# Kernel tuning notes

Measured on AMD Instinct MI355X. Metric: run time of the kernel, lower is better.

The kernel has to match this reference:

```python
import jax, jax.numpy as jnp
import numpy as np

B, T, N = 128, 32, 196
E = 1024   # embed dim
FD = 1024  # feature dim
H = 1024   # hidden size
A = 1024   # attention dim
SCALE = 0.02


def setup_inputs() -> dict:
    key = jax.random.key(0)
    ks = jax.random.split(key, 16)
    g = lambda k, shape: (jax.random.normal(k, shape, dtype=jnp.float32) * SCALE)
    return {
        "feats": jax.random.normal(ks[0], (B, N, FD), dtype=jnp.float32),
        "embeddings": jax.random.normal(ks[1], (B, T, E), dtype=jnp.float32),
        # additive attention params: v^T tanh(feats @ Wf + h @ Wh + b_att)
        "Wf": g(ks[2], (FD, A)),
        "Wh": g(ks[3], (H, A)),
        "b_att": jnp.zeros((A,), dtype=jnp.float32),
        "v": g(ks[4], (A,)),
        # layer-0 LSTMCell (input = concat(embed, attn) of size E+FD)
        "W_ih0": g(ks[5], (4 * H, E + FD)),
        "W_hh0": g(ks[6], (4 * H, H)),
        "b_ih0": jnp.zeros((4 * H,), dtype=jnp.float32),
        "b_hh0": jnp.zeros((4 * H,), dtype=jnp.float32),
        # layer-1 LSTMCell (input size H)
        "W_ih1": g(ks[7], (4 * H, H)),
        "W_hh1": g(ks[8], (4 * H, H)),
        "b_ih1": jnp.zeros((4 * H,), dtype=jnp.float32),
        "b_hh1": jnp.zeros((4 * H,), dtype=jnp.float32),
    }


def _lstm_cell(x, h, c, W_ih, W_hh, b_ih, b_hh):
    # PyTorch LSTMCell: gates ordered i, f, g, o
    gates = x @ W_ih.T + h @ W_hh.T + (b_ih + b_hh)
    i, f, g, o = jnp.split(gates, 4, axis=-1)
    c_new = jax.nn.sigmoid(f) * c + jax.nn.sigmoid(i) * jnp.tanh(g)
    h_new = jax.nn.sigmoid(o) * jnp.tanh(c_new)
    return h_new, c_new


def reference(feats, embeddings, Wf, Wh, b_att, v, W_ih0, W_hh0, b_ih0, b_hh0,
              W_ih1, W_hh1, b_ih1, b_hh1):
    Bb = embeddings.shape[0]
    # precompute the h-independent half of the attention energies: [B, N, A]
    f_proj = jnp.einsum("bnf,fa->bna", feats, Wf) + b_att

    h0 = jnp.zeros((Bb, H), dtype=feats.dtype)
    c0 = jnp.zeros((Bb, H), dtype=feats.dtype)

    def step(carry, embed_t):
        h0, c0 = carry
        # additive attention with query h0
        e = jnp.tanh(f_proj + (h0 @ Wh)[:, None, :])      # [B, N, A]
        scores = jnp.einsum("bna,a->bn", e, v)            # [B, N]
        alpha = jax.nn.softmax(scores, axis=-1)
        attn = jnp.einsum("bn,bnf->bf", alpha, feats)     # [B, FD]
        x = jnp.concatenate([embed_t, attn], axis=1)      # [B, E+FD]
        h0n, c0n = _lstm_cell(x, h0, c0, W_ih0, W_hh0, b_ih0, b_hh0)
        # faithful to source: layer 1 uses (h0n, c0n) as its state AND h0n as input
        h1, c1 = _lstm_cell(h0n, h0n, c0n, W_ih1, W_hh1, b_ih1, b_hh1)
        return (h0n, c0n), h1

    (_, _), outs = jax.lax.scan(step, (h0, c0), jnp.swapaxes(embeddings, 0, 1))
    return jnp.swapaxes(outs, 0, 1)  # [B, T, H]
```

## Files before the change

### kernel.cpp

```cpp
#include <hip/hip_runtime.h>
#include <hip/hip_cooperative_groups.h>
#include <cstddef>

typedef unsigned short ushort_t;
typedef unsigned int uint_t;
typedef __attribute__((ext_vector_type(8))) short bf16x8;
typedef __attribute__((ext_vector_type(4))) float f32x4;

constexpr int kB  = 128;
constexpr int kT  = 32;
constexpr int kN  = 196;
constexpr int kH  = 1024;

constexpr int ARENA_BYTES = 34816;

__device__ __forceinline__ float fsigmoid(float x) { return 1.f / (1.f + __expf(-x)); }
__device__ __forceinline__ float ftanh(float x)    { return 1.f - 2.f / (__expf(2.f * x) + 1.f); }
__device__ __forceinline__ ushort_t f2bf(float f) {
    uint_t u = __float_as_uint(f);
    return (ushort_t)((u + 0x7fffu + ((u >> 16) & 1u)) >> 16);
}

__global__ __launch_bounds__(256) void wf_transpose(
    const float* __restrict__ Wsrc, ushort_t* __restrict__ dst)
{
    __shared__ float t[64][65];
    const int k0 = blockIdx.x * 64, a0 = blockIdx.y * 64;
    const int c = threadIdx.x & 15, r0 = threadIdx.x >> 4;
#pragma unroll
    for (int i = 0; i < 4; ++i) {
        const int r = r0 + i * 16;
        const float4 v = *(const float4*)(Wsrc + (size_t)(k0 + r) * 1024 + a0 + c * 4);
        t[r][c * 4 + 0] = v.x; t[r][c * 4 + 1] = v.y;
        t[r][c * 4 + 2] = v.z; t[r][c * 4 + 3] = v.w;
    }
    __syncthreads();
#pragma unroll
    for (int i = 0; i < 4; ++i) {
        const int r = r0 + i * 16;
        ushort4 h;
        h.x = f2bf(t[c * 4 + 0][r]); h.y = f2bf(t[c * 4 + 1][r]);
        h.z = f2bf(t[c * 4 + 2][r]); h.w = f2bf(t[c * 4 + 3][r]);
        *(ushort4*)&dst[(size_t)(a0 + r) * 1024 + k0 + c * 4] = h;
    }
}

__global__ __launch_bounds__(256) void pack_whh0(
    const float* __restrict__ Whh0, ushort_t* __restrict__ Wbig)
{
    const int idx = blockIdx.x * 256 + threadIdx.x;
    const int j = idx >> 8, k4 = (idx & 255) * 4;
    const int u = j >> 2, g = j & 3;
    const float4 v = *(const float4*)(Whh0 + (size_t)(g * 1024 + u) * 1024 + k4);
    ushort4 h;
    h.x = f2bf(v.x); h.y = f2bf(v.y); h.z = f2bf(v.z); h.w = f2bf(v.w);
    *(ushort4*)&Wbig[(size_t)(1024 + j) * 1024 + k4] = h;
}

__global__ __launch_bounds__(256) void pack_w1sum(
    const float* __restrict__ Wih1, const float* __restrict__ Whh1,
    ushort_t* __restrict__ Wbig)
{
    const int idx = blockIdx.x * 256 + threadIdx.x;
    const int j = idx >> 8, k4 = (idx & 255) * 4;
    const int u = j >> 2, g = j & 3;
    const size_t o = (size_t)(g * 1024 + u) * 1024 + k4;
    const float4 a = *(const float4*)(Wih1 + o);
    const float4 b = *(const float4*)(Whh1 + o);
    ushort4 h;
    h.x = f2bf(a.x + b.x); h.y = f2bf(a.y + b.y);
    h.z = f2bf(a.z + b.z); h.w = f2bf(a.w + b.w);
    *(ushort4*)&Wbig[(size_t)(5120 + j) * 1024 + k4] = h;
}

__global__ __launch_bounds__(256) void pack_w0cat(
    const float* __restrict__ Wih0, ushort_t* __restrict__ W0cat)
{
    const int idx = blockIdx.x * 256 + threadIdx.x;
    const int j = idx >> 9, k4 = (idx & 511) * 4;
    const int u = j >> 2, g = j & 3;
    const int srccol = (k4 < 1024) ? (k4 + 1024) : (k4 - 1024);
    const float4 v = *(const float4*)(Wih0 + (size_t)(g * 1024 + u) * 2048 + srccol);
    ushort4 h;
    h.x = f2bf(v.x); h.y = f2bf(v.y); h.z = f2bf(v.z); h.w = f2bf(v.w);
    *(ushort4*)&W0cat[(size_t)j * 2048 + k4] = h;
}

__global__ __launch_bounds__(256) void cast_bf(
    const float* __restrict__ src, ushort_t* __restrict__ dst)
{
    const size_t idx = ((size_t)blockIdx.x * 256 + threadIdx.x) * 4;
    const float4 v = *(const float4*)(src + idx);
    ushort4 h;
    h.x = f2bf(v.x); h.y = f2bf(v.y); h.z = f2bf(v.z); h.w = f2bf(v.w);
    *(ushort4*)&dst[idx] = h;
}

template<int BF>
__global__ __launch_bounds__(256) void fproj_mfma(
    const float* __restrict__ featsf, const ushort_t* __restrict__ featsbf,
    const ushort_t* __restrict__ WfT,
    const float* __restrict__ bias, ushort_t* __restrict__ fprojbf)
{
    __shared__ alignas(16) char farena[40960];
    ushort_t* As = (ushort_t*)farena;
    ushort_t* Bs = As + 2 * 5120;
    ushort_t* Cs = (ushort_t*)farena;

    const int tid = threadIdx.x;
    const int n0 = blockIdx.x * 128, m0 = blockIdx.y * 128;
    const int lane = tid & 63, w = tid >> 6;
    const int wm = (w & 1) * 64, wn = (w >> 1) * 64;
    const int lr = lane & 15, quad = lane >> 4;

    const int xrow0 = tid >> 2, xrow1 = 64 + (tid >> 2);
    const int xkc = (tid & 3) * 8;

    f32x4 acc[4][4];
#pragma unroll
    for (int i = 0; i < 4; ++i)
#pragma unroll
        for (int j = 0; j < 4; ++j)
            acc[i][j] = (f32x4){0.f, 0.f, 0.f, 0.f};

    uint4 a0r, a1r, b0r, b1r;
    float4 f00, f01, f10, f11;

    auto LOAD = [&](int k0) {
        if (BF) {
            a0r = *(const uint4*)&featsbf[(size_t)(m0 + xrow0) * 1024 + k0 + xkc];
            a1r = *(const uint4*)&featsbf[(size_t)(m0 + xrow1) * 1024 + k0 + xkc];
        } else {
            f00 = *(const float4*)&featsf[(size_t)(m0 + xrow0) * 1024 + k0 + xkc];
            f01 = *(const float4*)&featsf[(size_t)(m0 + xrow0) * 1024 + k0 + xkc + 4];
            f10 = *(const float4*)&featsf[(size_t)(m0 + xrow1) * 1024 + k0 + xkc];
            f11 = *(const float4*)&featsf[(size_t)(m0 + xrow1) * 1024 + k0 + xkc + 4];
        }
        b0r = *(const uint4*)&WfT[(size_t)(n0 + xrow0) * 1024 + k0 + xkc];
        b1r = *(const uint4*)&WfT[(size_t)(n0 + xrow1) * 1024 + k0 + xkc];
    };
    auto WRITE = [&](int buf) {
        if (BF) {
            *(uint4*)&As[buf * 5120 + xrow0 * 40 + xkc] = a0r;
            *(uint4*)&As[buf * 5120 + xrow1 * 40 + xkc] = a1r;
        } else {
            ushort4 h;
            h.x = f2bf(f00.x); h.y = f2bf(f00.y); h.z = f2bf(f00.z); h.w = f2bf(f00.w);
            *(ushort4*)&As[buf * 5120 + xrow0 * 40 + xkc] = h;
            h.x = f2bf(f01.x); h.y = f2bf(f01.y); h.z = f2bf(f01.z); h.w = f2bf(f01.w);
            *(ushort4*)&As[buf * 5120 + xrow0 * 40 + xkc + 4] = h;
            h.x = f2bf(f10.x); h.y = f2bf(f10.y); h.z = f2bf(f10.z); h.w = f2bf(f10.w);
            *(ushort4*)&As[buf * 5120 + xrow1 * 40 + xkc] = h;
            h.x = f2bf(f11.x); h.y = f2bf(f11.y); h.z = f2bf(f11.z); h.w = f2bf(f11.w);
            *(ushort4*)&As[buf * 5120 + xrow1 * 40 + xkc + 4] = h;
        }
        *(uint4*)&Bs[buf * 5120 + xrow0 * 40 + xkc] = b0r;
        *(uint4*)&Bs[buf * 5120 + xrow1 * 40 + xkc] = b1r;
    };

    LOAD(0); WRITE(0); __syncthreads();
    int cur = 0;
    for (int k0 = 32; k0 <= 1024; k0 += 32) {
        const bool more = (k0 < 1024);
        if (more) LOAD(k0);
        bf16x8 af[4], bb[4];
#pragma unroll
        for (int mf = 0; mf < 4; ++mf)
            af[mf] = *(const bf16x8*)&As[cur * 5120 + (wm + mf * 16 + lr) * 40 + quad * 8];
#pragma unroll
        for (int nf = 0; nf < 4; ++nf)
            bb[nf] = *(const bf16x8*)&Bs[cur * 5120 + (wn + nf * 16 + lr) * 40 + quad * 8];
#pragma unroll
        for (int mf = 0; mf < 4; ++mf)
#pragma unroll
            for (int nf = 0; nf < 4; ++nf)
                acc[mf][nf] = __builtin_amdgcn_mfma_f32_16x16x32_bf16(
                    af[mf], bb[nf], acc[mf][nf], 0, 0, 0);
        if (more) WRITE(cur ^ 1);
        __syncthreads();
        cur ^= 1;
    }

#pragma unroll
    for (int nf = 0; nf < 4; ++nf) {
        const int n = wn + nf * 16 + lr;
        const float bn = bias[n0 + n];
#pragma unroll
        for (int mf = 0; mf < 4; ++mf)
#pragma unroll
            for (int r = 0; r < 4; ++r) {
                const int m = wm + mf * 16 + quad * 4 + r;
                Cs[m * 136 + n] = f2bf(acc[mf][nf][r] + bn);
            }
    }
    __syncthreads();
#pragma unroll
    for (int p = 0; p < 8; ++p) {
        const int row = p * 16 + (tid >> 4);
        const int c8 = (tid & 15) * 8;
        const uint4 v = *(const uint4*)&Cs[row * 136 + c8];
        *(uint4*)&fprojbf[(size_t)(m0 + row) * 1024 + n0 + c8] = v;
    }
}

__device__ __forceinline__ void phase_hgemm(
    char* arena, int job, int tstep,
    const ushort_t* __restrict__ hbf, const ushort_t* __restrict__ Wbig,
    const float* __restrict__ cbuf,
    const float* __restrict__ bih1, const float* __restrict__ bhh1,
    float* __restrict__ hwh, float* __restrict__ Ypart,
    float* __restrict__ out)
{
    ushort_t* xs  = (ushort_t*)arena;
    ushort_t* wsB = xs + 10240;
    float*    eps = (float*)arena;

    const int tid = threadIdx.x;
    const int n0 = job * 64;
    const int lane = tid & 63, w = tid >> 6;
    const int wm = (w & 1) * 64, wn = (w >> 1) * 32;
    const int lr = lane & 15, quad = lane >> 4;

    const int xrow0 = tid >> 2, xrow1 = 64 + (tid >> 2);
    const int xkc = (tid & 3) * 8;

    f32x4 acc[4][2];
#pragma unroll
    for (int i = 0; i < 4; ++i) {
        acc[i][0] = (f32x4){0.f, 0.f, 0.f, 0.f};
        acc[i][1] = (f32x4){0.f, 0.f, 0.f, 0.f};
    }

    uint4 x0r, x1r, w0r;
    auto LOAD = [&](int k0) {
        x0r = *(const uint4*)&hbf[(size_t)xrow0 * 1024 + k0 + xkc];
        x1r = *(const uint4*)&hbf[(size_t)xrow1 * 1024 + k0 + xkc];
        w0r = *(const uint4*)&Wbig[(size_t)(n0 + xrow0) * 1024 + k0 + xkc];
    };
    auto WRITE = [&](int buf) {
        *(uint4*)&xs[buf * 5120 + xrow0 * 40 + xkc] = x0r;
        *(uint4*)&xs[buf * 5120 + xrow1 * 40 + xkc] = x1r;
        *(uint4*)&wsB[buf * 2560 + xrow0 * 40 + xkc] = w0r;
    };

    LOAD(0); WRITE(0); __syncthreads();
    int cur = 0;
    for (int k0 = 32; k0 <= 1024; k0 += 32) {
        const bool more = (k0 < 1024);
        if (more) LOAD(k0);
        bf16x8 af[4], bb[2];
#pragma unroll
        for (int mf = 0; mf < 4; ++mf)
            af[mf] = *(const bf16x8*)&xs[cur * 5120 + (wm + mf * 16 + lr) * 40 + quad * 8];
#pragma unroll
        for (int nf = 0; nf < 2; ++nf)
            bb[nf] = *(const bf16x8*)&wsB[cur * 2560 + (wn + nf * 16 + lr) * 40 + quad * 8];
#pragma unroll
        for (int mf = 0; mf < 4; ++mf)
#pragma unroll
            for (int nf = 0; nf < 2; ++nf)
                acc[mf][nf] = __builtin_amdgcn_mfma_f32_16x16x32_bf16(
                    af[mf], bb[nf], acc[mf][nf], 0, 0, 0);
        if (more) WRITE(cur ^ 1);
        __syncthreads();
        cur ^= 1;
    }

    if (n0 < 5120) {
        float* dst = (n0 < 1024) ? hwh : Ypart;
        const int stride = (n0 < 1024) ? 1024 : 4096;
        const int nbase = (n0 < 1024) ? n0 : (n0 - 1024);
#pragma unroll
        for (int mf = 0; mf < 4; ++mf)
#pragma unroll
            for (int nf = 0; nf < 2; ++nf)
#pragma unroll
                for (int r = 0; r < 4; ++r) {
                    const int m = wm + mf * 16 + quad * 4 + r;
                    const int n = nbase + wn + nf * 16 + lr;
                    dst[(size_t)m * stride + n] = acc[mf][nf][r];
                }
    } else {
#pragma unroll
        for (int mf = 0; mf < 4; ++mf)
#pragma unroll
            for (int nf = 0; nf < 2; ++nf)
#pragma unroll
                for (int r = 0; r < 4; ++r)
                    eps[(wm + mf * 16 + quad * 4 + r) * 65 + (wn + nf * 16 + lr)] = acc[mf][nf][r];
        __syncthreads();
        if (tstep >= 1) {
#pragma unroll
            for (int i = 0; i < 8; ++i) {
                const int cid = i * 256 + tid;
                const int b = cid & 127, ulc = cid >> 7;
                const int u = ((n0 - 5120) >> 2) + ulc;
                const float iv = fsigmoid(eps[b * 65 + ulc * 4 + 0] + bih1[u]        + bhh1[u]);
                const float fv = fsigmoid(eps[b * 65 + ulc * 4 + 1] + bih1[1024 + u] + bhh1[1024 + u]);
                const float gv = ftanh   (eps[b * 65 + ulc * 4 + 2] + bih1[2048 + u] + bhh1[2048 + u]);
                const float ov = fsigmoid(eps[b * 65 + ulc * 4 + 3] + bih1[3072 + u] + bhh1[3072 + u]);
                const float cp = cbuf[(size_t)b * 1024 + u];
                const float cn = fv * cp + iv * gv;
                out[((size_t)b * kT + (tstep - 1)) * 1024 + u] = ov * ftanh(cn);
            }
        }
    }
}

__device__ __forceinline__ void phase_scores(
    int job,
    const ushort_t* __restrict__ fprojbf, const float* __restrict__ hwh,
    const float* __restrict__ vvec, float* __restrict__ scoresbuf)
{
    const int b = job & 127, chunk = job >> 7;
    const int tid = threadIdx.x, lane = tid & 63, w = tid >> 6;

    float hw[16], vr[16];
    {
        const int a0 = lane * 16;
#pragma unroll
        for (int q = 0; q < 4; ++q) {
            const float4 s0 = *(const float4*)(hwh + (size_t)b * 1024 + a0 + q * 4);
            hw[q * 4 + 0] = s0.x; hw[q * 4 + 1] = s0.y;
            hw[q * 4 + 2] = s0.z; hw[q * 4 + 3] = s0.w;
            const float4 vv = *(const float4*)(vvec + a0 + q * 4);
            vr[q * 4 + 0] = vv.x; vr[q * 4 + 1] = vv.y;
            vr[q * 4 + 2] = vv.z; vr[q * 4 + 3] = vv.w;
        }
    }

#pragma unroll
    for (int i = 0; i < 7; ++i) {
        const int n = chunk * 28 + w * 7 + i;
        const ushort_t* fp = fprojbf + ((size_t)(b * kN + n)) * 1024 + lane * 16;
        const uint4 u0 = *(const uint4*)(fp);
        const uint4 u1 = *(const uint4*)(fp + 8);
        float p = 0.f;
        const uint_t uu[8] = {u0.x, u0.y, u0.z, u0.w, u1.x, u1.y, u1.z, u1.w};
#pragma unroll
        for (int q = 0; q < 8; ++q) {
            const float xa = __uint_as_float(uu[q] << 16);
            const float xb = __uint_as_float(uu[q] & 0xffff0000u);
            p += ftanh(xa + hw[2 * q]) * vr[2 * q];
            p += ftanh(xb + hw[2 * q + 1]) * vr[2 * q + 1];
        }
#pragma unroll
        for (int off = 32; off; off >>= 1) p += __shfl_down(p, off);
        if (lane == 0) scoresbuf[b * kN + n] = p;
    }
}

__device__ __forceinline__ void phase_attn(
    char* arena, int job,
    const float* __restrict__ scoresbuf, const ushort_t* __restrict__ featsbf,
    ushort_t* __restrict__ attnbf)
{
    float* alpha_s = (float*)arena;
    float* red = alpha_s + 200;
    const int b = job >> 1;
    const int tid = threadIdx.x;

    const float val = (tid < kN) ? scoresbuf[b * kN + tid] : -1e30f;
    float m = val;
#pragma unroll
    for (int off = 32; off; off >>= 1) m = fmaxf(m, __shfl_down(m, off));
    if ((tid & 63) == 0) red[tid >> 6] = m;
    __syncthreads();
    m = fmaxf(fmaxf(red[0], red[1]), fmaxf(red[2], red[3]));
    const float e = (tid < kN) ? __expf(val - m) : 0.f;
    float s = e;
#pragma unroll
    for (int off = 32; off; off >>= 1) s += __shfl_down(s, off);
    if ((tid & 63) == 0) red[4 + (tid >> 6)] = s;
    __syncthreads();
    s = red[4] + red[5] + red[6] + red[7];
    if (tid < kN) alpha_s[tid] = e * (1.f / s);
    __syncthreads();

    const int f0 = (job & 1) * 512 + tid * 2;
    const ushort_t* fb = featsbf + (size_t)b * kN * 1024 + f0;
    float a0 = 0.f, a1 = 0.f;
#pragma unroll 4
    for (int n = 0; n < kN; ++n) {
        const uint_t u = *(const uint_t*)(fb + (size_t)n * 1024);
        a0 += alpha_s[n] * __uint_as_float(u << 16);
        a1 += alpha_s[n] * __uint_as_float(u & 0xffff0000u);
    }
    uint_t o = ((uint_t)f2bf(a1) << 16) | (uint_t)f2bf(a0);
    *(uint_t*)&attnbf[(size_t)b * 1024 + f0] = o;
}

__device__ __forceinline__ void phase_gates(
    char* arena, int job, int tstep,
    const ushort_t* __restrict__ attnbf, const ushort_t* __restrict__ embbf,
    const ushort_t* __restrict__ W0cat, const float* __restrict__ Ypart,
    const float* __restrict__ bih0, const float* __restrict__ bhh0,
    float* __restrict__ cbuf, ushort_t* __restrict__ hbf)
{
    ushort_t* xs  = (ushort_t*)arena;
    ushort_t* ws2 = xs + 10240;
    float*    eps = (float*)arena;

    const int tid = threadIdx.x;
    const int n0 = job * 32;
    const int lane = tid & 63, w = tid >> 6;
    const int wm = (w & 1) * 64, wn = (w >> 1) * 16;
    const int lr = lane & 15, quad = lane >> 4;

    const int xrow0 = tid >> 2, xrow1 = 64 + (tid >> 2);
    const int xkc = (tid & 3) * 8;
    const int wrow = tid >> 3, wkc = (tid & 7) * 4;

    f32x4 acc[4];
#pragma unroll
    for (int i = 0; i < 4; ++i) acc[i] = (f32x4){0.f, 0.f, 0.f, 0.f};

    uint4 x0r, x1r; uint2 w0r;
    auto LOAD = [&](int k0) {
        const ushort_t* s0 = (k0 < 1024)
            ? (attnbf + (size_t)xrow0 * 1024 + k0)
            : (embbf + ((size_t)xrow0 * kT + tstep) * 1024 + (k0 - 1024));
        const ushort_t* s1 = (k0 < 1024)
            ? (attnbf + (size_t)xrow1 * 1024 + k0)
            : (embbf + ((size_t)xrow1 * kT + tstep) * 1024 + (k0 - 1024));
        x0r = *(const uint4*)(s0 + xkc);
        x1r = *(const uint4*)(s1 + xkc);
        w0r = *(const uint2*)&W0cat[(size_t)(n0 + wrow) * 2048 + k0 + wkc];
    };
    auto WRITE = [&](int buf) {
        *(uint4*)&xs[buf * 5120 + xrow0 * 40 + xkc] = x0r;
        *(uint4*)&xs[buf * 5120 + xrow1 * 40 + xkc] = x1r;
        *(uint2*)&ws2[buf * 1280 + wrow * 40 + wkc] = w0r;
    };

    LOAD(0); WRITE(0); __syncthreads();
    int cur = 0;
    for (int k0 = 32; k0 <= 2048; k0 += 32) {
        const bool more = (k0 < 2048);
        if (more) LOAD(k0);
        bf16x8 af[4], bb;
#pragma unroll
        for (int mf = 0; mf < 4; ++mf)
            af[mf] = *(const bf16x8*)&xs[cur * 5120 + (wm + mf * 16 + lr) * 40 + quad * 8];
        bb = *(const bf16x8*)&ws2[cur * 1280 + (wn + lr) * 40 + quad * 8];
#pragma unroll
        for (int mf = 0; mf < 4; ++mf)
            acc[mf] = __builtin_amdgcn_mfma_f32_16x16x32_bf16(
                af[mf], bb, acc[mf], 0, 0, 0);
        if (more) WRITE(cur ^ 1);
        __syncthreads();
        cur ^= 1;
    }

#pragma unroll
    for (int mf = 0; mf < 4; ++mf)
#pragma unroll
        for (int r = 0; r < 4; ++r)
            eps[(wm + mf * 16 + quad * 4 + r) * 33 + wn + lr] = acc[mf][r];
    __syncthreads();

#pragma unroll
    for (int i = 0; i < 4; ++i) {
        const int cid = i * 256 + tid;
        const int b = cid & 127, ulc = cid >> 7;
        const int u = (n0 >> 2) + ulc;
        const int jb = n0 + ulc * 4;
        const float* yp = Ypart + (size_t)b * 4096 + jb;
        const float iv = fsigmoid(eps[b * 33 + ulc * 4 + 0] + yp[0] + bih0[u]        + bhh0[u]);
        const float fv = fsigmoid(eps[b * 33 + ulc * 4 + 1] + yp[1] + bih0[1024 + u] + bhh0[1024 + u]);
        const float gv = ftanh   (eps[b * 33 + ulc * 4 + 2] + yp[2] + bih0[2048 + u] + bhh0[2048 + u]);
        const float ov = fsigmoid(eps[b * 33 + ulc * 4 + 3] + yp[3] + bih0[3072 + u] + bhh0[3072 + u]);
        const float cp = cbuf[(size_t)b * 1024 + u];
        const float cn = fv * cp + iv * gv;
        cbuf[(size_t)b * 1024 + u] = cn;
        hbf[(size_t)b * 1024 + u] = f2bf(ov * ftanh(cn));
    }
}

__global__ __launch_bounds__(256) void hgemm_A(
    const ushort_t* __restrict__ hbf, const ushort_t* __restrict__ Wbig,
    const float* __restrict__ cbuf,
    const float* __restrict__ bih1, const float* __restrict__ bhh1,
    float* __restrict__ hwh, float* __restrict__ Ypart,
    float* __restrict__ out, int tstep)
{
    __shared__ alignas(16) char arena[ARENA_BYTES];
    phase_hgemm(arena, blockIdx.x, tstep, hbf, Wbig, cbuf, bih1, bhh1, hwh, Ypart, out);
}

__global__ __launch_bounds__(256) void scores_kernel(
    const ushort_t* __restrict__ fprojbf, const float* __restrict__ hwh,
    const float* __restrict__ vvec, float* __restrict__ scoresbuf)
{
    phase_scores(blockIdx.x + 128 * blockIdx.y, fprojbf, hwh, vvec, scoresbuf);
}

template<int BF>
__global__ __launch_bounds__(256) void attn_kernel(
    const float* __restrict__ scoresbuf, const float* __restrict__ featsf,
    const ushort_t* __restrict__ featsbf, ushort_t* __restrict__ attnbf)
{
    __shared__ float alpha_s[200];
    __shared__ float red[8];
    const int b = blockIdx.x;
    const int tid = threadIdx.x;

    const float val = (tid < kN) ? scoresbuf[b * kN + tid] : -1e30f;
    float m = val;
#pragma unroll
    for (int off = 32; off; off >>= 1) m = fmaxf(m, __shfl_down(m, off));
    if ((tid & 63) == 0) red[tid >> 6] = m;
    __syncthreads();
    m = fmaxf(fmaxf(red[0], red[1]), fmaxf(red[2], red[3]));
    const float e = (tid < kN) ? __expf(val - m) : 0.f;
    float s = e;
#pragma unroll
    for (int off = 32; off; off >>= 1) s += __shfl_down(s, off);
    if ((tid & 63) == 0) red[4 + (tid >> 6)] = s;
    __syncthreads();
    s = red[4] + red[5] + red[6] + red[7];
    if (tid < kN) alpha_s[tid] = e * (1.f / s);
    __syncthreads();

    if (BF) {
        const int f0 = blockIdx.y * 512 + tid * 2;
        const ushort_t* fb = featsbf + (size_t)b * kN * 1024 + f0;
        float a0 = 0.f, a1 = 0.f;
#pragma unroll 4
        for (int n = 0; n < kN; ++n) {
            const uint_t u = *(const uint_t*)(fb + (size_t)n * 1024);
            a0 += alpha_s[n] * __uint_as_float(u << 16);
            a1 += alpha_s[n] * __uint_as_float(u & 0xffff0000u);
        }
        uint_t o = ((uint_t)f2bf(a1) << 16) | (uint_t)f2bf(a0);
        *(uint_t*)&attnbf[(size_t)b * 1024 + f0] = o;
    } else {
        const int f = blockIdx.y * 256 + tid;
        const float* fb = featsf + (size_t)b * kN * 1024 + f;
        float a = 0.f;
#pragma unroll 4
        for (int n = 0; n < kN; ++n) a += alpha_s[n] * fb[(size_t)n * 1024];
        attnbf[(size_t)b * 1024 + f] = f2bf(a);
    }
}

__global__ __launch_bounds__(256) void gatesC(
    const ushort_t* __restrict__ attnbf, const ushort_t* __restrict__ embbf,
    const ushort_t* __restrict__ W0cat, const float* __restrict__ Ypart,
    const float* __restrict__ bih0, const float* __restrict__ bhh0,
    float* __restrict__ cbuf, ushort_t* __restrict__ hbf, int tstep)
{
    __shared__ alignas(16) char arena[ARENA_BYTES];
    phase_gates(arena, blockIdx.x, tstep, attnbf, embbf, W0cat, Ypart,
                bih0, bhh0, cbuf, hbf);
}

__global__ __launch_bounds__(256, 2) void mega_kernel(
    ushort_t* hbf, const ushort_t* Wbig, float* cbuf,
    const float* bih1, const float* bhh1,
    float* hwh, float* Ypart, float* out,
    const ushort_t* fprojbf, const float* vvec, float* scoresbuf,
    const ushort_t* featsbf, ushort_t* attnbf,
    const ushort_t* embbf, const ushort_t* W0cat,
    const float* bih0, const float* bhh0)
{
    __shared__ alignas(16) char arena[ARENA_BYTES];
    cooperative_groups::grid_group grid = cooperative_groups::this_grid();
    const int blk = blockIdx.x;

    for (int t = 0; t < kT; ++t) {
        if (blk < 144)
            phase_hgemm(arena, blk, t, hbf, Wbig, cbuf, bih1, bhh1, hwh, Ypart, out);
        grid.sync();
        for (int j = blk; j < 896; j += 512)
            phase_scores(j, fprojbf, hwh, vvec, scoresbuf);
        grid.sync();
        if (blk < 256)
            phase_attn(arena, blk, scoresbuf, featsbf, attnbf);
        grid.sync();
        if (blk < 128)
            phase_gates(arena, blk, t, attnbf, embbf, W0cat, Ypart,
                        bih0, bhh0, cbuf, hbf);
        grid.sync();
    }
    if (blk < 64)
        phase_hgemm(arena, 80 + blk, kT, hbf, Wbig, cbuf, bih1, bhh1, hwh, Ypart, out);
}

extern "C" void kernel_launch(void* const* d_in, const int* in_sizes, int n_in,
                              void* d_out, int out_size, void* d_ws, size_t ws_size,
                              hipStream_t stream)
{
    const float* feats = (const float*)d_in[0];
    const float* emb   = (const float*)d_in[1];
    const float* Wf    = (const float*)d_in[2];
    const float* Wh    = (const float*)d_in[3];
    const float* b_att = (const float*)d_in[4];
    const float* vvec  = (const float*)d_in[5];
    const float* Wih0  = (const float*)d_in[6];
    const float* Whh0  = (const float*)d_in[7];
    const float* bih0  = (const float*)d_in[8];
    const float* bhh0  = (const float*)d_in[9];
    const float* Wih1  = (const float*)d_in[10];
    const float* Whh1  = (const float*)d_in[11];
    const float* bih1  = (const float*)d_in[12];
    const float* bhh1  = (const float*)d_in[13];
    float* out = (float*)d_out;

    ushort_t* fprojbf = (ushort_t*)d_ws;
    ushort_t* embbf   = fprojbf + (size_t)25088 * 1024;
    ushort_t* Wbig    = embbf   + (size_t)4096 * 1024;
    ushort_t* W0cat   = Wbig    + (size_t)9216 * 1024;
    ushort_t* WfT     = W0cat   + (size_t)4096 * 2048;
    ushort_t* hbf     = WfT     + (size_t)1024 * 1024;
    ushort_t* attnbf  = hbf     + (size_t)128 * 1024;
    float* hwh        = (float*)(attnbf + (size_t)128 * 1024);
    float* Ypart      = hwh   + (size_t)128 * 1024;
    float* cbuf       = Ypart + (size_t)128 * 4096;
    float* scoresbuf  = cbuf  + (size_t)128 * 1024;
    ushort_t* featsbf = (ushort_t*)(scoresbuf + 128 * 196);

    const size_t need_full = 152668160;
    const bool use_bf = (ws_size >= need_full);

    hipMemsetAsync(hbf, 0, sizeof(ushort_t) * 128 * 1024, stream);
    hipMemsetAsync(cbuf, 0, sizeof(float) * 128 * 1024, stream);

    wf_transpose<<<dim3(16, 16), 256, 0, stream>>>(Wf, WfT);
    wf_transpose<<<dim3(16, 16), 256, 0, stream>>>(Wh, Wbig);
    pack_whh0<<<4096, 256, 0, stream>>>(Whh0, Wbig);
    pack_w1sum<<<4096, 256, 0, stream>>>(Wih1, Whh1, Wbig);
    pack_w0cat<<<8192, 256, 0, stream>>>(Wih0, W0cat);
    cast_bf<<<4096, 256, 0, stream>>>(emb, embbf);
    if (use_bf) cast_bf<<<25088, 256, 0, stream>>>(feats, featsbf);

    if (use_bf)
        fproj_mfma<1><<<dim3(8, 196), 256, 0, stream>>>(feats, featsbf, WfT, b_att, fprojbf);
    else
        fproj_mfma<0><<<dim3(8, 196), 256, 0, stream>>>(feats, featsbf, WfT, b_att, fprojbf);

    bool did_coop = false;
    if (use_bf) {
        static int coop_ok = -1;
        if (coop_ok < 0) {
            int dev = 0; (void)hipGetDevice(&dev);
            int coop = 0;
            (void)hipDeviceGetAttribute(&coop, hipDeviceAttributeCooperativeLaunch, dev);
            int ncu = 0;
            (void)hipDeviceGetAttribute(&ncu, hipDeviceAttributeMultiprocessorCount, dev);
            int maxb = 0;
            hipError_t oe = hipOccupancyMaxActiveBlocksPerMultiprocessor(
                &maxb, mega_kernel, 256, 0);
            coop_ok = (coop != 0 && oe == hipSuccess && (long)maxb * ncu >= 512) ? 1 : 0;
        }
        if (coop_ok) {
            void* kargs[] = {
                (void*)&hbf, (void*)&Wbig, (void*)&cbuf, (void*)&bih1, (void*)&bhh1,
                (void*)&hwh, (void*)&Ypart, (void*)&out, (void*)&fprojbf, (void*)&vvec,
                (void*)&scoresbuf, (void*)&featsbf, (void*)&attnbf, (void*)&embbf,
                (void*)&W0cat, (void*)&bih0, (void*)&bhh0 };
            hipError_t le = hipLaunchCooperativeKernel(
                mega_kernel, dim3(512), dim3(256), kargs, 0u, stream);
            did_coop = (le == hipSuccess);
        }
    }

    if (!did_coop) {
        for (int t = 0; t < kT; ++t) {
            hgemm_A<<<144, 256, 0, stream>>>(hbf, Wbig, cbuf, bih1, bhh1,
                                             hwh, Ypart, out, t);
            scores_kernel<<<dim3(128, 7), 256, 0, stream>>>(fprojbf, hwh, vvec, scoresbuf);
            if (use_bf)
                attn_kernel<1><<<dim3(128, 2), 256, 0, stream>>>(scoresbuf, feats, featsbf, attnbf);
            else
                attn_kernel<0><<<dim3(128, 4), 256, 0, stream>>>(scoresbuf, feats, featsbf, attnbf);
            gatesC<<<128, 256, 0, stream>>>(attnbf, embbf, W0cat, Ypart,
                                            bih0, bhh0, cbuf, hbf, t);
        }
        hgemm_A<<<144, 256, 0, stream>>>(hbf, Wbig, cbuf, bih1, bhh1,
                                         hwh, Ypart, out, kT);
    }

    (void)in_sizes; (void)n_in; (void)out_size; (void)ws_size;
}
```

Before: 3.225 ms.

## Precompute embedding gate projections and replace cooperative megakernel with per-step launches

Adds a batched MFMA GEMM that computes the embedding half of the layer-0 input projection for all timesteps at once. The per-step gates kernel then runs only over the attention half (K=1024) and adds the precomputed values. The cooperative grid-synced megakernel is removed in favour of four ordinary kernel launches per step. The final step launches only the 64 blocks needed for the layer-1 output. This lowers per-step GEMM work and grid-sync cost, but adds launch overhead and a 64MB fp32 workspace buffer that is used only if the workspace is large enough.

```diff
diff --git a/kernel.cpp b/kernel.cpp
--- a/kernel.cpp
+++ b/kernel.cpp
@@ -1,5 +1,4 @@
 #include <hip/hip_runtime.h>
-#include <hip/hip_cooperative_groups.h>
 #include <cstddef>
 
 typedef unsigned short ushort_t;
@@ -203,6 +202,79 @@
     }
 }
 
+__global__ __launch_bounds__(256) void yemb_mfma(
+    const ushort_t* __restrict__ embbf, const ushort_t* __restrict__ W0cat,
+    float* __restrict__ Yemb)
+{
+    __shared__ alignas(16) char farena[40960];
+    ushort_t* As = (ushort_t*)farena;
+    ushort_t* Bs = As + 2 * 5120;
+
+    const int tid = threadIdx.x;
+    const int n0 = blockIdx.x * 128, m0 = blockIdx.y * 128;
+    const int lane = tid & 63, w = tid >> 6;
+    const int wm = (w & 1) * 64, wn = (w >> 1) * 64;
+    const int lr = lane & 15, quad = lane >> 4;
+
+    const int xrow0 = tid >> 2, xrow1 = 64 + (tid >> 2);
+    const int xkc = (tid & 3) * 8;
+
+    f32x4 acc[4][4];
+#pragma unroll
+    for (int i = 0; i < 4; ++i)
+#pragma unroll
+        for (int j = 0; j < 4; ++j)
+            acc[i][j] = (f32x4){0.f, 0.f, 0.f, 0.f};
+
+    uint4 a0r, a1r, b0r, b1r;
+    auto LOAD = [&](int k0) {
+        a0r = *(const uint4*)&embbf[(size_t)(m0 + xrow0) * 1024 + k0 + xkc];
+        a1r = *(const uint4*)&embbf[(size_t)(m0 + xrow1) * 1024 + k0 + xkc];
+        b0r = *(const uint4*)&W0cat[(size_t)(n0 + xrow0) * 2048 + 1024 + k0 + xkc];
+        b1r = *(const uint4*)&W0cat[(size_t)(n0 + xrow1) * 2048 + 1024 + k0 + xkc];
+    };
+    auto WRITE = [&](int buf) {
+        *(uint4*)&As[buf * 5120 + xrow0 * 40 + xkc] = a0r;
+        *(uint4*)&As[buf * 5120 + xrow1 * 40 + xkc] = a1r;
+        *(uint4*)&Bs[buf * 5120 + xrow0 * 40 + xkc] = b0r;
+        *(uint4*)&Bs[buf * 5120 + xrow1 * 40 + xkc] = b1r;
+    };
+
+    LOAD(0); WRITE(0); __syncthreads();
+    int cur = 0;
+    for (int k0 = 32; k0 <= 1024; k0 += 32) {
+        const bool more = (k0 < 1024);
+        if (more) LOAD(k0);
+        bf16x8 af[4], bb[4];
+#pragma unroll
+        for (int mf = 0; mf < 4; ++mf)
+            af[mf] = *(const bf16x8*)&As[cur * 5120 + (wm + mf * 16 + lr) * 40 + quad * 8];
+#pragma unroll
+        for (int nf = 0; nf < 4; ++nf)
+            bb[nf] = *(const bf16x8*)&Bs[cur * 5120 + (wn + nf * 16 + lr) * 40 + quad * 8];
+#pragma unroll
+        for (int mf = 0; mf < 4; ++mf)
+#pragma unroll
+            for (int nf = 0; nf < 4; ++nf)
+                acc[mf][nf] = __builtin_amdgcn_mfma_f32_16x16x32_bf16(
+                    af[mf], bb[nf], acc[mf][nf], 0, 0, 0);
+        if (more) WRITE(cur ^ 1);
+        __syncthreads();
+        cur ^= 1;
+    }
+
+#pragma unroll
+    for (int mf = 0; mf < 4; ++mf)
+#pragma unroll
+        for (int nf = 0; nf < 4; ++nf)
+#pragma unroll
+            for (int r = 0; r < 4; ++r) {
+                const int m = m0 + wm + mf * 16 + quad * 4 + r;
+                const int n = n0 + wn + nf * 16 + lr;
+                Yemb[(size_t)m * 4096 + n] = acc[mf][nf][r];
+            }
+}
+
 __device__ __forceinline__ void phase_hgemm(
     char* arena, int job, int tstep,
     const ushort_t* __restrict__ hbf, const ushort_t* __restrict__ Wbig,
@@ -307,12 +379,23 @@
     }
 }
 
-__device__ __forceinline__ void phase_scores(
-    int job,
+__global__ __launch_bounds__(256) void hgemm_A(
+    const ushort_t* __restrict__ hbf, const ushort_t* __restrict__ Wbig,
+    const float* __restrict__ cbuf,
+    const float* __restrict__ bih1, const float* __restrict__ bhh1,
+    float* __restrict__ hwh, float* __restrict__ Ypart,
+    float* __restrict__ out, int tstep, int job_base)
+{
+    __shared__ alignas(16) char arena[ARENA_BYTES];
+    phase_hgemm(arena, blockIdx.x + job_base, tstep, hbf, Wbig, cbuf,
+                bih1, bhh1, hwh, Ypart, out);
+}
+
+__global__ __launch_bounds__(256) void scores_kernel(
     const ushort_t* __restrict__ fprojbf, const float* __restrict__ hwh,
     const float* __restrict__ vvec, float* __restrict__ scoresbuf)
 {
-    const int b = job & 127, chunk = job >> 7;
+    const int b = blockIdx.x, chunk = blockIdx.y;
     const int tid = threadIdx.x, lane = tid & 63, w = tid >> 6;
 
     float hw[16], vr[16];
@@ -348,151 +431,6 @@
         for (int off = 32; off; off >>= 1) p += __shfl_down(p, off);
         if (lane == 0) scoresbuf[b * kN + n] = p;
     }
-}
-
-__device__ __forceinline__ void phase_attn(
-    char* arena, int job,
-    const float* __restrict__ scoresbuf, const ushort_t* __restrict__ featsbf,
-    ushort_t* __restrict__ attnbf)
-{
-    float* alpha_s = (float*)arena;
-    float* red = alpha_s + 200;
-    const int b = job >> 1;
-    const int tid = threadIdx.x;
-
-    const float val = (tid < kN) ? scoresbuf[b * kN + tid] : -1e30f;
-    float m = val;
-#pragma unroll
-    for (int off = 32; off; off >>= 1) m = fmaxf(m, __shfl_down(m, off));
-    if ((tid & 63) == 0) red[tid >> 6] = m;
-    __syncthreads();
-    m = fmaxf(fmaxf(red[0], red[1]), fmaxf(red[2], red[3]));
-    const float e = (tid < kN) ? __expf(val - m) : 0.f;
-    float s = e;
-#pragma unroll
-    for (int off = 32; off; off >>= 1) s += __shfl_down(s, off);
-    if ((tid & 63) == 0) red[4 + (tid >> 6)] = s;
-    __syncthreads();
-    s = red[4] + red[5] + red[6] + red[7];
-    if (tid < kN) alpha_s[tid] = e * (1.f / s);
-    __syncthreads();
-
-    const int f0 = (job & 1) * 512 + tid * 2;
-    const ushort_t* fb = featsbf + (size_t)b * kN * 1024 + f0;
-    float a0 = 0.f, a1 = 0.f;
-#pragma unroll 4
-    for (int n = 0; n < kN; ++n) {
-        const uint_t u = *(const uint_t*)(fb + (size_t)n * 1024);
-        a0 += alpha_s[n] * __uint_as_float(u << 16);
-        a1 += alpha_s[n] * __uint_as_float(u & 0xffff0000u);
-    }
-    uint_t o = ((uint_t)f2bf(a1) << 16) | (uint_t)f2bf(a0);
-    *(uint_t*)&attnbf[(size_t)b * 1024 + f0] = o;
-}
-
-__device__ __forceinline__ void phase_gates(
-    char* arena, int job, int tstep,
-    const ushort_t* __restrict__ attnbf, const ushort_t* __restrict__ embbf,
-    const ushort_t* __restrict__ W0cat, const float* __restrict__ Ypart,
-    const float* __restrict__ bih0, const float* __restrict__ bhh0,
-    float* __restrict__ cbuf, ushort_t* __restrict__ hbf)
-{
-    ushort_t* xs  = (ushort_t*)arena;
-    ushort_t* ws2 = xs + 10240;
-    float*    eps = (float*)arena;
-
-    const int tid = threadIdx.x;
-    const int n0 = job * 32;
-    const int lane = tid & 63, w = tid >> 6;
-    const int wm = (w & 1) * 64, wn = (w >> 1) * 16;
-    const int lr = lane & 15, quad = lane >> 4;
-
-    const int xrow0 = tid >> 2, xrow1 = 64 + (tid >> 2);
-    const int xkc = (tid & 3) * 8;
-    const int wrow = tid >> 3, wkc = (tid & 7) * 4;
-
-    f32x4 acc[4];
-#pragma unroll
-    for (int i = 0; i < 4; ++i) acc[i] = (f32x4){0.f, 0.f, 0.f, 0.f};
-
-    uint4 x0r, x1r; uint2 w0r;
-    auto LOAD = [&](int k0) {
-        const ushort_t* s0 = (k0 < 1024)
-            ? (attnbf + (size_t)xrow0 * 1024 + k0)
-            : (embbf + ((size_t)xrow0 * kT + tstep) * 1024 + (k0 - 1024));
-        const ushort_t* s1 = (k0 < 1024)
-            ? (attnbf + (size_t)xrow1 * 1024 + k0)
-            : (embbf + ((size_t)xrow1 * kT + tstep) * 1024 + (k0 - 1024));
-        x0r = *(const uint4*)(s0 + xkc);
-        x1r = *(const uint4*)(s1 + xkc);
-        w0r = *(const uint2*)&W0cat[(size_t)(n0 + wrow) * 2048 + k0 + wkc];
-    };
-    auto WRITE = [&](int buf) {
-        *(uint4*)&xs[buf * 5120 + xrow0 * 40 + xkc] = x0r;
-        *(uint4*)&xs[buf * 5120 + xrow1 * 40 + xkc] = x1r;
-        *(uint2*)&ws2[buf * 1280 + wrow * 40 + wkc] = w0r;
-    };
-
-    LOAD(0); WRITE(0); __syncthreads();
-    int cur = 0;
-    for (int k0 = 32; k0 <= 2048; k0 += 32) {
-        const bool more = (k0 < 2048);
-        if (more) LOAD(k0);
-        bf16x8 af[4], bb;
-#pragma unroll
-        for (int mf = 0; mf < 4; ++mf)
-            af[mf] = *(const bf16x8*)&xs[cur * 5120 + (wm + mf * 16 + lr) * 40 + quad * 8];
-        bb = *(const bf16x8*)&ws2[cur * 1280 + (wn + lr) * 40 + quad * 8];
-#pragma unroll
-        for (int mf = 0; mf < 4; ++mf)
-            acc[mf] = __builtin_amdgcn_mfma_f32_16x16x32_bf16(
-                af[mf], bb, acc[mf], 0, 0, 0);
-        if (more) WRITE(cur ^ 1);
-        __syncthreads();
-        cur ^= 1;
-    }
-
-#pragma unroll
-    for (int mf = 0; mf < 4; ++mf)
-#pragma unroll
-        for (int r = 0; r < 4; ++r)
-            eps[(wm + mf * 16 + quad * 4 + r) * 33 + wn + lr] = acc[mf][r];
-    __syncthreads();
-
-#pragma unroll
-    for (int i = 0; i < 4; ++i) {
-        const int cid = i * 256 + tid;
-        const int b = cid & 127, ulc = cid >> 7;
-        const int u = (n0 >> 2) + ulc;
-        const int jb = n0 + ulc * 4;
-        const float* yp = Ypart + (size_t)b * 4096 + jb;
-        const float iv = fsigmoid(eps[b * 33 + ulc * 4 + 0] + yp[0] + bih0[u]        + bhh0[u]);
-        const float fv = fsigmoid(eps[b * 33 + ulc * 4 + 1] + yp[1] + bih0[1024 + u] + bhh0[1024 + u]);
-        const float gv = ftanh   (eps[b * 33 + ulc * 4 + 2] + yp[2] + bih0[2048 + u] + bhh0[2048 + u]);
-        const float ov = fsigmoid(eps[b * 33 + ulc * 4 + 3] + yp[3] + bih0[3072 + u] + bhh0[3072 + u]);
-        const float cp = cbuf[(size_t)b * 1024 + u];
-        const float cn = fv * cp + iv * gv;
-        cbuf[(size_t)b * 1024 + u] = cn;
-        hbf[(size_t)b * 1024 + u] = f2bf(ov * ftanh(cn));
-    }
-}
-
-__global__ __launch_bounds__(256) void hgemm_A(
-    const ushort_t* __restrict__ hbf, const ushort_t* __restrict__ Wbig,
-    const float* __restrict__ cbuf,
-    const float* __restrict__ bih1, const float* __restrict__ bhh1,
-    float* __restrict__ hwh, float* __restrict__ Ypart,
-    float* __restrict__ out, int tstep)
-{
-    __shared__ alignas(16) char arena[ARENA_BYTES];
-    phase_hgemm(arena, blockIdx.x, tstep, hbf, Wbig, cbuf, bih1, bhh1, hwh, Ypart, out);
-}
-
-__global__ __launch_bounds__(256) void scores_kernel(
-    const ushort_t* __restrict__ fprojbf, const float* __restrict__ hwh,
-    const float* __restrict__ vvec, float* __restrict__ scoresbuf)
-{
-    phase_scores(blockIdx.x + 128 * blockIdx.y, fprojbf, hwh, vvec, scoresbuf);
 }
 
 template<int BF>
@@ -544,47 +482,116 @@
     }
 }
 
+template<int EMB>
+__device__ __forceinline__ void phase_gates(
+    char* arena, int job, int tstep,
+    const ushort_t* __restrict__ attnbf, const ushort_t* __restrict__ embbf,
+    const ushort_t* __restrict__ W0cat, const float* __restrict__ Ypart,
+    const float* __restrict__ Yemb,
+    const float* __restrict__ bih0, const float* __restrict__ bhh0,
+    float* __restrict__ cbuf, ushort_t* __restrict__ hbf)
+{
+    ushort_t* xs  = (ushort_t*)arena;
+    ushort_t* ws2 = xs + 10240;
+    float*    eps = (float*)arena;
+
+    const int tid = threadIdx.x;
+    const int n0 = job * 32;
+    const int lane = tid & 63, w = tid >> 6;
+    const int wm = (w & 1) * 64, wn = (w >> 1) * 16;
+    const int lr = lane & 15, quad = lane >> 4;
+
+    const int xrow0 = tid >> 2, xrow1 = 64 + (tid >> 2);
+    const int xkc = (tid & 3) * 8;
+    const int wrow = tid >> 3, wkc = (tid & 7) * 4;
+
+    constexpr int KMAX = EMB ? 2048 : 1024;
+
+    f32x4 acc[4];
+#pragma unroll
+    for (int i = 0; i < 4; ++i) acc[i] = (f32x4){0.f, 0.f, 0.f, 0.f};
+
+    uint4 x0r, x1r; uint2 w0r;
+    auto LOAD = [&](int k0) {
+        const ushort_t* s0 = (!EMB || k0 < 1024)
+            ? (attnbf + (size_t)xrow0 * 1024 + k0)
+            : (embbf + ((size_t)xrow0 * kT + tstep) * 1024 + (k0 - 1024));
+        const ushort_t* s1 = (!EMB || k0 < 1024)
+            ? (attnbf + (size_t)xrow1 * 1024 + k0)
+            : (embbf + ((size_t)xrow1 * kT + tstep) * 1024 + (k0 - 1024));
+        x0r = *(const uint4*)(s0 + xkc);
+        x1r = *(const uint4*)(s1 + xkc);
+        w0r = *(const uint2*)&W0cat[(size_t)(n0 + wrow) * 2048 + k0 + wkc];
+    };
+    auto WRITE = [&](int buf) {
+        *(uint4*)&xs[buf * 5120 + xrow0 * 40 + xkc] = x0r;
+        *(uint4*)&xs[buf * 5120 + xrow1 * 40 + xkc] = x1r;
+        *(uint2*)&ws2[buf * 1280 + wrow * 40 + wkc] = w0r;
+    };
+
+    LOAD(0); WRITE(0); __syncthreads();
+    int cur = 0;
+    for (int k0 = 32; k0 <= KMAX; k0 += 32) {
+        const bool more = (k0 < KMAX);
+        if (more) LOAD(k0);
+        bf16x8 af[4], bb;
+#pragma unroll
+        for (int mf = 0; mf < 4; ++mf)
+            af[mf] = *(const bf16x8*)&xs[cur * 5120 + (wm + mf * 16 + lr) * 40 + quad * 8];
+        bb = *(const bf16x8*)&ws2[cur * 1280 + (wn + lr) * 40 + quad * 8];
+#pragma unroll
+        for (int mf = 0; mf < 4; ++mf)
+            acc[mf] = __builtin_amdgcn_mfma_f32_16x16x32_bf16(
+                af[mf], bb, acc[mf], 0, 0, 0);
+        if (more) WRITE(cur ^ 1);
+        __syncthreads();
+        cur ^= 1;
+    }
+
+#pragma unroll
+    for (int mf = 0; mf < 4; ++mf)
+#pragma unroll
+        for (int r = 0; r < 4; ++r)
+            eps[(wm + mf * 16 + quad * 4 + r) * 33 + wn + lr] = acc[mf][r];
+    __syncthreads();
+
+#pragma unroll
+    for (int i = 0; i < 4; ++i) {
+        const int cid = i * 256 + tid;
+        const int b = cid & 127, ulc = cid >> 7;
+        const int u = (n0 >> 2) + ulc;
+        const int jb = n0 + ulc * 4;
+        const float* yp = Ypart + (size_t)b * 4096 + jb;
+        float e0 = eps[b * 33 + ulc * 4 + 0] + yp[0];
+        float e1 = eps[b * 33 + ulc * 4 + 1] + yp[1];
+        float e2 = eps[b * 33 + ulc * 4 + 2] + yp[2];
+        float e3 = eps[b * 33 + ulc * 4 + 3] + yp[3];
+        if (!EMB) {
+            const float* ye = Yemb + ((size_t)b * kT + tstep) * 4096 + jb;
+            e0 += ye[0]; e1 += ye[1]; e2 += ye[2]; e3 += ye[3];
+        }
+        const float iv = fsigmoid(e0 + bih0[u]        + bhh0[u]);
+        const float fv = fsigmoid(e1 + bih0[1024 + u] + bhh0[1024 + u]);
+        const float gv = ftanh   (e2 + bih0[2048 + u] + bhh0[2048 + u]);
+        const float ov = fsigmoid(e3 + bih0[3072 + u] + bhh0[3072 + u]);
+        const float cp = cbuf[(size_t)b * 1024 + u];
+        const float cn = fv * cp + iv * gv;
+        cbuf[(size_t)b * 1024 + u] = cn;
+        hbf[(size_t)b * 1024 + u] = f2bf(ov * ftanh(cn));
+    }
+}
+
+template<int EMB>
 __global__ __launch_bounds__(256) void gatesC(
     const ushort_t* __restrict__ attnbf, const ushort_t* __restrict__ embbf,
     const ushort_t* __restrict__ W0cat, const float* __restrict__ Ypart,
+    const float* __restrict__ Yemb,
     const float* __restrict__ bih0, const float* __restrict__ bhh0,
     float* __restrict__ cbuf, ushort_t* __restrict__ hbf, int tstep)
 {
     __shared__ alignas(16) char arena[ARENA_BYTES];
-    phase_gates(arena, blockIdx.x, tstep, attnbf, embbf, W0cat, Ypart,
-                bih0, bhh0, cbuf, hbf);
-}
-
-__global__ __launch_bounds__(256, 2) void mega_kernel(
-    ushort_t* hbf, const ushort_t* Wbig, float* cbuf,
-    const float* bih1, const float* bhh1,
-    float* hwh, float* Ypart, float* out,
-    const ushort_t* fprojbf, const float* vvec, float* scoresbuf,
-    const ushort_t* featsbf, ushort_t* attnbf,
-    const ushort_t* embbf, const ushort_t* W0cat,
-    const float* bih0, const float* bhh0)
-{
-    __shared__ alignas(16) char arena[ARENA_BYTES];
-    cooperative_groups::grid_group grid = cooperative_groups::this_grid();
-    const int blk = blockIdx.x;
-
-    for (int t = 0; t < kT; ++t) {
-        if (blk < 144)
-            phase_hgemm(arena, blk, t, hbf, Wbig, cbuf, bih1, bhh1, hwh, Ypart, out);
-        grid.sync();
-        for (int j = blk; j < 896; j += 512)
-            phase_scores(j, fprojbf, hwh, vvec, scoresbuf);
-        grid.sync();
-        if (blk < 256)
-            phase_attn(arena, blk, scoresbuf, featsbf, attnbf);
-        grid.sync();
-        if (blk < 128)
-            phase_gates(arena, blk, t, attnbf, embbf, W0cat, Ypart,
-                        bih0, bhh0, cbuf, hbf);
-        grid.sync();
-    }
-    if (blk < 64)
-        phase_hgemm(arena, 80 + blk, kT, hbf, Wbig, cbuf, bih1, bhh1, hwh, Ypart, out);
+    phase_gates<EMB>(arena, blockIdx.x, tstep, attnbf, embbf, W0cat, Ypart,
+                     Yemb, bih0, bhh0, cbuf, hbf);
 }
 
 extern "C" void kernel_launch(void* const* d_in, const int* in_sizes, int n_in,
@@ -619,9 +626,12 @@
     float* cbuf       = Ypart + (size_t)128 * 4096;
     float* scoresbuf  = cbuf  + (size_t)128 * 1024;
     ushort_t* featsbf = (ushort_t*)(scoresbuf + 128 * 196);
+    float* Yemb       = (float*)(featsbf + (size_t)25088 * 1024);
 
     const size_t need_full = 152668160;
-    const bool use_bf = (ws_size >= need_full);
+    const size_t need_yemb = need_full + (size_t)4096 * 4096 * 4;
+    const bool use_bf   = (ws_size >= need_full);
+    const bool use_yemb = use_bf && (ws_size >= need_yemb);
 
     hipMemsetAsync(hbf, 0, sizeof(ushort_t) * 128 * 1024, stream);
     hipMemsetAsync(cbuf, 0, sizeof(float) * 128 * 1024, stream);
@@ -639,47 +649,26 @@
     else
         fproj_mfma<0><<<dim3(8, 196), 256, 0, stream>>>(feats, featsbf, WfT, b_att, fprojbf);
 
-    bool did_coop = false;
-    if (use_bf) {
-        static int coop_ok = -1;
-        if (coop_ok < 0) {
-            int dev = 0; (void)hipGetDevice(&dev);
-            int coop = 0;
-            (void)hipDeviceGetAttribute(&coop, hipDeviceAttributeCooperativeLaunch, dev);
-            int ncu = 0;
-            (void)hipDeviceGetAttribute(&ncu, hipDeviceAttributeMultiprocessorCount, dev);
-            int maxb = 0;
-            hipError_t oe = hipOccupancyMaxActiveBlocksPerMultiprocessor(
-                &maxb, mega_kernel, 256, 0);
-            coop_ok = (coop != 0 && oe == hipSuccess && (long)maxb * ncu >= 512) ? 1 : 0;
-        }
-        if (coop_ok) {
-            void* kargs[] = {
-                (void*)&hbf, (void*)&Wbig, (void*)&cbuf, (void*)&bih1, (void*)&bhh1,
-                (void*)&hwh, (void*)&Ypart, (void*)&out, (void*)&fprojbf, (void*)&vvec,
-                (void*)&scoresbuf, (void*)&featsbf, (void*)&attnbf, (void*)&embbf,
-                (void*)&W0cat, (void*)&bih0, (void*)&bhh0 };
-            hipError_t le = hipLaunchCooperativeKernel(
-                mega_kernel, dim3(512), dim3(256), kargs, 0u, stream);
-            did_coop = (le == hipSuccess);
-        }
-    }
-
-    if (!did_coop) {
-        for (int t = 0; t < kT; ++t) {
-            hgemm_A<<<144, 256, 0, stream>>>(hbf, Wbig, cbuf, bih1, bhh1,
-                                             hwh, Ypart, out, t);
-            scores_kernel<<<dim3(128, 7), 256, 0, stream>>>(fprojbf, hwh, vvec, scoresbuf);
-            if (use_bf)
-                attn_kernel<1><<<dim3(128, 2), 256, 0, stream>>>(scoresbuf, feats, featsbf, attnbf);
-            else
-                attn_kernel<0><<<dim3(128, 4), 256, 0, stream>>>(scoresbuf, feats, featsbf, attnbf);
-            gatesC<<<128, 256, 0, stream>>>(attnbf, embbf, W0cat, Ypart,
-                                            bih0, bhh0, cbuf, hbf, t);
-        }
+    if (use_yemb)
+        yemb_mfma<<<dim3(32, 32), 256, 0, stream>>>(embbf, W0cat, Yemb);
+
+    for (int t = 0; t < kT; ++t) {
         hgemm_A<<<144, 256, 0, stream>>>(hbf, Wbig, cbuf, bih1, bhh1,
-                                         hwh, Ypart, out, kT);
-    }
+                                         hwh, Ypart, out, t, 0);
+        scores_kernel<<<dim3(128, 7), 256, 0, stream>>>(fprojbf, hwh, vvec, scoresbuf);
+        if (use_bf)
+            attn_kernel<1><<<dim3(128, 2), 256, 0, stream>>>(scoresbuf, feats, featsbf, attnbf);
+        else
+            attn_kernel<0><<<dim3(128, 4), 256, 0, stream>>>(scoresbuf, feats, featsbf, attnbf);
+        if (use_yemb)
+            gatesC<0><<<128, 256, 0, stream>>>(attnbf, embbf, W0cat, Ypart, Yemb,
+                                               bih0, bhh0, cbuf, hbf, t);
+        else
+            gatesC<1><<<128, 256, 0, stream>>>(attnbf, embbf, W0cat, Ypart, Yemb,
+                                               bih0, bhh0, cbuf, hbf, t);
+    }
+    hgemm_A<<<64, 256, 0, stream>>>(hbf, Wbig, cbuf, bih1, bhh1,
+                                    hwh, Ypart, out, kT, 80);
 
     (void)in_sizes; (void)n_in; (void)out_size; (void)ws_size;
 }
```

New measurement: 2.954 ms. -8.4%, faster.
